# Performance work log

Hardware: AMD Instinct MI355X
Metric: run time of the kernel (lower is better)

The kernel has to match this reference:

```python
import jax, jax.numpy as jnp
import numpy as np

EPS = 1e-7          # keras backend epsilon
BN_EPS = 1e-3       # keras BatchNormalization default epsilon
SCALES = (2, 4, 8, 16, 32)  # 2**i for i in 1..max_scale, max_scale=5


def _box_filter(x, k):
    # depthwise conv with all-ones k x k kernel, SAME padding (TF semantics)
    c = x.shape[-1]
    kern = jnp.ones((k, k, 1, c), x.dtype)
    return jax.lax.conv_general_dilated(
        x, kern, (1, 1), 'SAME',
        dimension_numbers=('NHWC', 'HWIO', 'NHWC'),
        feature_group_count=c)


def setup_inputs() -> dict:
    key = jax.random.key(0)
    ks = jax.random.split(key, 4)
    B, H, W, C, R = 16, 56, 56, 128, 8
    x = jax.random.normal(ks[0], (B, H, W, C), jnp.float32)
    kappa = jax.random.uniform(ks[1], (len(SCALES),), jnp.float32, -0.5, 0.5)
    W1 = jax.random.normal(ks[2], (C, C // R), jnp.float32) * (1.0 / np.sqrt(C))
    b1 = jnp.zeros((C // R,), jnp.float32)
    W2 = jax.random.normal(ks[3], (C // R, C), jnp.float32) * (1.0 / np.sqrt(C // R))
    b2 = jnp.zeros((C,), jnp.float32)
    gamma = jnp.ones((C,), jnp.float32)
    beta = jnp.zeros((C,), jnp.float32)
    bn_mean = jnp.zeros((C,), jnp.float32)
    bn_var = jnp.ones((C,), jnp.float32)
    return dict(x=x, kappa=kappa, W1=W1, b1=b1, W2=W2, b2=b2,
                gamma=gamma, beta=beta, bn_mean=bn_mean, bn_var=bn_var)


def reference(x, kappa, W1, b1, W2, b2, gamma, beta, bn_mean, bn_var):
    # per-sample min-max scaling over (H, W, C)
    xmin = jnp.min(x, axis=(1, 2, 3), keepdims=True)
    xmax = jnp.max(x, axis=(1, 2, 3), keepdims=True)
    xs = (x - xmin) / (xmax - xmin + EPS)

    # multi-scale box measures: [B,H,W,C,S]
    measures = jnp.stack([_box_filter(xs, k) for k in SCALES], axis=-1)
    log_m = jnp.log(measures + EPS)
    log_r = jnp.log(jnp.asarray(SCALES, jnp.float32))  # [S]

    # OLS slope of log_m vs log_r along scale axis -> alphas [B,H,W,C]
    xc = log_r - jnp.mean(log_r)
    alphas = jnp.sum(log_m * xc, axis=-1) / jnp.sum(xc * xc)

    # squeeze-and-excite on alphas
    squeeze = jnp.mean(alphas, axis=(1, 2))            # [B,C]
    hidden = jax.nn.relu(squeeze @ W1 + b1)            # [B,C//r]
    excite = jax.nn.sigmoid(hidden @ W2 + b2)          # [B,C]

    # weighted OLS estimate: alpha * (log_k + log_r) -> [B,H,W,C,S]
    k_ = jax.nn.sigmoid(kappa)
    log_k = jax.nn.sigmoid(jnp.log(k_ + EPS))          # [S]
    wols = alphas[..., None] * (log_k + log_r)

    # standardized (mean-centered) cosine similarity along scale axis, in [0,1]
    a = log_m - jnp.mean(log_m, axis=-1, keepdims=True)
    b = wols - jnp.mean(wols, axis=-1, keepdims=True)
    cos = jnp.sum(a * b, axis=-1) / (
        jnp.linalg.norm(a, axis=-1) * jnp.linalg.norm(b, axis=-1) + EPS)
    sim = 0.5 * (cos + 1.0)                            # [B,H,W,C]

    # inference-mode batchnorm on alphas
    alpha_norm = gamma * (alphas - bn_mean) * jax.lax.rsqrt(bn_var + BN_EPS) + beta

    x_exc = xs * excite[:, None, None, :]
    return sim * jax.nn.sigmoid(alpha_norm) + (1.0 - sim) * x_exc
```

## Files before the change

kernel.cpp:

```cpp
#include <hip/hip_runtime.h>
#include <hip/hip_fp16.h>

#define NTOT   6422528
#define NPERB  401408
#define NQ4    100352
#define LOG2E  1.4426950408889634f

__device__ __forceinline__ float sigmoidf_fast(float x) {
    return __builtin_amdgcn_rcpf(1.f + __expf(-x));
}

__device__ __forceinline__ void kappa_consts(const float* kap, float* dcs) {
    float v[5]; float mean = 0.f;
    for (int s = 0; s < 5; s++) {
        float lr = 0.6931471805599453f * (float)(s + 1);
        float k_ = 1.f / (1.f + expf(-kap[s]));
        float lk = 1.f / (1.f + expf(-logf(k_ + 1e-7f)));
        v[s] = lk + lr; mean += v[s];
    }
    mean *= 0.2f; float nd = 0.f;
    for (int s = 0; s < 5; s++) { float d = v[s] - mean; dcs[s] = d; nd += d * d; }
    dcs[5] = sqrtf(nd);
}

struct ScaleU { int rb1, rb0; float xmch; };

__global__ void k_minmax(const float4* __restrict__ x4,
                         float* __restrict__ pmxp, float* __restrict__ pmnp,
                         float* __restrict__ sq) {
    int p = blockIdx.x;
    int b = p & 15, chunk = p >> 4;
    if (chunk == 0) {
        for (int k = threadIdx.x; k < 128; k += 256) sq[b * 128 + k] = 0.f;
    }
    const float4* base = x4 + b * NQ4 + chunk * 1568;
    float mx = -3.4e38f, mn = 3.4e38f;
    for (int q = threadIdx.x; q < 1568; q += 256) {
        float4 v = base[q];
        mx = fmaxf(mx, fmaxf(fmaxf(v.x, v.y), fmaxf(v.z, v.w)));
        mn = fminf(mn, fminf(fminf(v.x, v.y), fminf(v.z, v.w)));
    }
    __shared__ float rmx[4], rmn[4];
    int lane = threadIdx.x & 63, w = threadIdx.x >> 6;
#pragma unroll
    for (int off = 32; off; off >>= 1) {
        mx = fmaxf(mx, __shfl_down(mx, off));
        mn = fminf(mn, __shfl_down(mn, off));
    }
    if (lane == 0) { rmx[w] = mx; rmn[w] = mn; }
    __syncthreads();
    if (threadIdx.x == 0) {
        mx = fmaxf(fmaxf(rmx[0], rmx[1]), fmaxf(rmx[2], rmx[3]));
        mn = fminf(fminf(rmn[0], rmn[1]), fminf(rmn[2], rmn[3]));
        pmxp[b * 64 + chunk] = mx;
        pmnp[b * 64 + chunk] = mn;
    }
}

__launch_bounds__(448, 7)
__global__ void k_satg(const float* __restrict__ x,   const float* __restrict__ kap,
                       const float* __restrict__ gam, const float* __restrict__ bet,
                       const float* __restrict__ bnm, const float* __restrict__ bnv,
                       const float* __restrict__ pmxp, const float* __restrict__ pmnp,
                       float* __restrict__ sq, unsigned int* __restrict__ ABu) {
    __shared__ float2 SAT2[57 * 57];
    __shared__ float2 tot2[448];
    __shared__ float  wsum[14];
    __shared__ float  cst[9];

    const int p = blockIdx.x;
    const int b = p & 15, cg = p >> 4;
    const int c0 = cg * 2;
    const int t = threadIdx.x;
    const int pos = t % 56;
    const int seg = t / 56;

    if (t < 57) SAT2[t] = make_float2(0.f, 0.f);
    if (t >= 64 && t < 120) SAT2[(t - 63) * 57] = make_float2(0.f, 0.f);
    if (t == 128) {
        float d[6]; kappa_consts(kap, d);
#pragma unroll
        for (int s2 = 0; s2 < 6; s2++) cst[s2] = d[s2];
    }

    float2 v[7];
    {
        const float2* xp = (const float2*)(x + b * NPERB + seg * 7 * 7168 + pos * 128 + c0);
        float2 acc = make_float2(0.f, 0.f);
#pragma unroll
        for (int k = 0; k < 7; k++) {
            float2 xv = xp[k * 3584];
            acc.x += xv.x; acc.y += xv.y;
            v[k] = acc;
        }
        tot2[t] = acc;
    }
    __syncthreads();
    if (t < 64) {
        float mxv = pmxp[b * 64 + t];
        float mnv = pmnp[b * 64 + t];
#pragma unroll
        for (int off = 32; off; off >>= 1) {
            mxv = fmaxf(mxv, __shfl_down(mxv, off));
            mnv = fminf(mnv, __shfl_down(mnv, off));
        }
        if (t == 0) {
            float xi = 1.f / (mxv - mnv + 1e-7f);
            cst[6] = mnv; cst[7] = xi; cst[8] = mnv * xi;
        }
    }
    {
        float2 base = make_float2(0.f, 0.f);
        for (int s = 0; s < seg; s++) {
            float2 tv = tot2[s * 56 + pos];
            base.x += tv.x; base.y += tv.y;
        }
#pragma unroll
        for (int k = 0; k < 7; k++)
            SAT2[(seg * 7 + 1 + k) * 57 + (pos + 1)] =
                make_float2(base.x + v[k].x, base.y + v[k].y);
    }
    __syncthreads();

    {
        const int rbase = (pos + 1) * 57 + seg * 7 + 1;
#pragma unroll
        for (int k = 0; k < 7; k++) v[k] = SAT2[rbase + k];
#pragma unroll
        for (int k = 1; k < 7; k++) { v[k].x += v[k - 1].x; v[k].y += v[k - 1].y; }
        tot2[seg * 56 + pos] = v[6];
    }
    __syncthreads();
    {
        float2 base = make_float2(0.f, 0.f);
        for (int s = 0; s < seg; s++) {
            float2 tv = tot2[s * 56 + pos];
            base.x += tv.x; base.y += tv.y;
        }
        const int rbase = (pos + 1) * 57 + seg * 7 + 1;
#pragma unroll
        for (int k = 0; k < 7; k++)
            SAT2[rbase + k] = make_float2(base.x + v[k].x, base.y + v[k].y);
    }
    __syncthreads();

    float asx = 0.f, asy = 0.f;
    {
        const int i = pos;
        const int j0 = seg * 7;
        const float xm = cst[6], xi = cst[7], xmxi = cst[8];
        const float d0 = cst[0], d1 = cst[1], d2 = cst[2], d3 = cst[3], d4 = cst[4], nd = cst[5];
        float C1x, C0x, C1y, C0y;
        {
            float g = gam[c0], be = bet[c0], bm = bnm[c0];
            float rsv = rsqrtf(bnv[c0] + 1e-3f);
            C1x = -(g * rsv) * (LOG2E * 0.1f);
            C0x = -(be - g * bm * rsv) * LOG2E;
            g = gam[c0 + 1]; be = bet[c0 + 1]; bm = bnm[c0 + 1];
            rsv = rsqrtf(bnv[c0 + 1] + 1e-3f);
            C1y = -(g * rsv) * (LOG2E * 0.1f);
            C0y = -(be - g * bm * rsv) * LOG2E;
        }

        auto mkU = [&](int hk) {
            ScaleU uu;
            int y1g = min(i + hk, 55) + 1;
            int y0g = max(i - hk + 1, 0);
            uu.rb1 = y1g * 57; uu.rb0 = y0g * 57;
            uu.xmch = xm * (float)(y1g - y0g);
            return uu;
        };
        const ScaleU u0 = mkU(1), u1 = mkU(2), u2 = mkU(4), u3 = mkU(8), u4 = mkU(16);

        auto meas = [&](int j, const ScaleU& uu, int hk) -> float2 {
            int x1g = min(j + hk, 55) + 1;
            int x0g = max(j - hk + 1, 0);
            float cw = (float)(x1g - x0g);
            float2 a = SAT2[uu.rb1 + x1g], bq = SAT2[uu.rb0 + x1g];
            float2 cq = SAT2[uu.rb1 + x0g], dq = SAT2[uu.rb0 + x0g];
            float sx = a.x - bq.x - cq.x + dq.x;
            float sy = a.y - bq.y - cq.y + dq.y;
            float tx = fmaf(-uu.xmch, cw, sx);
            float ty = fmaf(-uu.xmch, cw, sy);
            float2 r;
            r.x = __log2f(fmaxf(fmaf(tx, xi, 1e-7f), 1e-7f));
            r.y = __log2f(fmaxf(fmaf(ty, xi, 1e-7f), 1e-7f));
            return r;
        };

        const float2* xrow = (const float2*)(x + b * NPERB + i * 7168 + c0);
        uint2* abrow = (uint2*)(ABu + b * NPERB + i * 7168 + c0);
#pragma unroll 2
        for (int jj = 0; jj < 7; jj++) {
            int j = j0 + jj;
            float2 l0 = meas(j, u0, 1);
            float2 l1 = meas(j, u1, 2);
            float2 l2 = meas(j, u2, 4);
            float2 l3 = meas(j, u3, 8);
            float2 l4 = meas(j, u4, 16);
            float2 xv = xrow[j * 64];
            uint2 outw;
            {
                float w2 = -2.f * l0.x - l1.x + l3.x + 2.f * l4.x;
                asx += w2;
                float alphas = w2 * 0.1f;
                float mean = 0.2f * (l0.x + l1.x + l2.x + l3.x + l4.x);
                float a0 = l0.x - mean, a1 = l1.x - mean, a2 = l2.x - mean,
                      a3 = l3.x - mean, a4 = l4.x - mean;
                float na2  = a0 * a0 + a1 * a1 + a2 * a2 + a3 * a3 + a4 * a4;
                float adot = a0 * d0 + a1 * d1 + a2 * d2 + a3 * d3 + a4 * d4;
                float na = __builtin_amdgcn_sqrtf(na2);
                float cosv = (alphas * adot) *
                             __builtin_amdgcn_rcpf(na * fabsf(alphas) * nd + 1e-7f);
                float sim = 0.5f * (cosv + 1.f);
                float sbn = __builtin_amdgcn_rcpf(1.f + exp2f(C1x * w2 + C0x));
                float xs = fmaf(xv.x, xi, -xmxi);
                outw.x = __builtin_bit_cast(unsigned int,
                          __floats2half2_rn(sim * sbn, (1.f - sim) * xs));
            }
            {
                float w2 = -2.f * l0.y - l1.y + l3.y + 2.f * l4.y;
                asy += w2;
                float alphas = w2 * 0.1f;
                float mean = 0.2f * (l0.y + l1.y + l2.y + l3.y + l4.y);
                float a0 = l0.y - mean, a1 = l1.y - mean, a2 = l2.y - mean,
                      a3 = l3.y - mean, a4 = l4.y - mean;
                float na2  = a0 * a0 + a1 * a1 + a2 * a2 + a3 * a3 + a4 * a4;
                float adot = a0 * d0 + a1 * d1 + a2 * d2 + a3 * d3 + a4 * d4;
                float na = __builtin_amdgcn_sqrtf(na2);
                float cosv = (alphas * adot) *
                             __builtin_amdgcn_rcpf(na * fabsf(alphas) * nd + 1e-7f);
                float sim = 0.5f * (cosv + 1.f);
                float sbn = __builtin_amdgcn_rcpf(1.f + exp2f(C1y * w2 + C0y));
                float xs = fmaf(xv.y, xi, -xmxi);
                outw.y = __builtin_bit_cast(unsigned int,
                          __floats2half2_rn(sim * sbn, (1.f - sim) * xs));
            }
            abrow[j * 64] = outw;
        }
    }
#pragma unroll
    for (int off = 32; off; off >>= 1) {
        asx += __shfl_down(asx, off);
        asy += __shfl_down(asy, off);
    }
    if ((t & 63) == 0) { wsum[(t >> 6) * 2] = asx; wsum[(t >> 6) * 2 + 1] = asy; }
    __syncthreads();
    if (t < 2) {
        float s = 0.f;
#pragma unroll
        for (int w = 0; w < 7; w++) s += wsum[w * 2 + t];
        atomicAdd(&sq[b * 128 + c0 + t], s * 0.1f);
    }
}

__launch_bounds__(256)
__global__ void k_mix(const unsigned int* __restrict__ ABu, const float* __restrict__ sq,
                      const float* __restrict__ W1, const float* __restrict__ b1,
                      const float* __restrict__ W2, const float* __restrict__ b2,
                      float* __restrict__ out) {
    __shared__ float sqz[128];
    __shared__ float hidp[256];
    __shared__ float hid[16];
    __shared__ float exc[128];
    int p = blockIdx.x;
    int b = p & 15, chunk = p >> 4;
    int tid = threadIdx.x;
    if (tid < 128) sqz[tid] = sq[b * 128 + tid] * (1.f / 3136.f);
    __syncthreads();
    {
        int h = tid & 15, g = tid >> 4;
        float acc = 0.f;
#pragma unroll
        for (int k = 0; k < 8; k++) {
            int c2 = g * 8 + k;
            acc += sqz[c2] * W1[c2 * 16 + h];
        }
        hidp[tid] = acc;
    }
    __syncthreads();
    if (tid < 16) {
        float acc = b1[tid];
#pragma unroll
        for (int g = 0; g < 16; g++) acc += hidp[g * 16 + tid];
        hid[tid] = fmaxf(acc, 0.f);
    }
    __syncthreads();
    if (tid < 128) {
        float acc = b2[tid];
#pragma unroll
        for (int h = 0; h < 16; h++) acc += hid[h] * W2[h * 128 + tid];
        exc[tid] = sigmoidf_fast(acc);
    }
    __syncthreads();
    const uint4* ab4 = (const uint4*)ABu + b * NQ4 + chunk * 784;
    float4* out4 = (float4*)out + b * NQ4 + chunk * 784;
    for (int q = tid; q < 784; q += 256) {
        int cb = ((chunk * 784 + q) & 31) << 2;
        uint4 u = ab4[q];
        float2 p0 = __half22float2(__builtin_bit_cast(__half2, u.x));
        float2 p1 = __half22float2(__builtin_bit_cast(__half2, u.y));
        float2 p2 = __half22float2(__builtin_bit_cast(__half2, u.z));
        float2 p3 = __half22float2(__builtin_bit_cast(__half2, u.w));
        out4[q] = make_float4(p0.x + p0.y * exc[cb],
                              p1.x + p1.y * exc[cb + 1],
                              p2.x + p2.y * exc[cb + 2],
                              p3.x + p3.y * exc[cb + 3]);
    }
}

extern "C" void kernel_launch(void* const* d_in, const int* in_sizes, int n_in,
                              void* d_out, int out_size, void* d_ws, size_t ws_size,
                              hipStream_t stream) {
    const float* x   = (const float*)d_in[0];
    const float* kap = (const float*)d_in[1];
    const float* W1  = (const float*)d_in[2];
    const float* b1  = (const float*)d_in[3];
    const float* W2  = (const float*)d_in[4];
    const float* b2  = (const float*)d_in[5];
    const float* gam = (const float*)d_in[6];
    const float* bet = (const float*)d_in[7];
    const float* bnm = (const float*)d_in[8];
    const float* bnv = (const float*)d_in[9];
    float* out = (float*)d_out;

    float* sq   = (float*)d_ws;
    float* pmxp = sq + 2048;
    float* pmnp = pmxp + 1024;
    unsigned* ABu = (unsigned*)(pmnp + 1024);

    k_minmax<<<1024, 256, 0, stream>>>((const float4*)x, pmxp, pmnp, sq);
    k_satg<<<1024, 448, 0, stream>>>(x, kap, gam, bet, bnm, bnv, pmxp, pmnp, sq, ABu);
    k_mix<<<2048, 256, 0, stream>>>(ABu, sq, W1, b1, W2, b2, out);
}
```

Baseline: 143.1 us.

## Transpose intermediate buffer to channel-pair-major layout and recover x from SAT

The intermediate half2 buffer is stored channel-pair-major with pixels ordered column-major, so k_satg's per-thread stores become contiguous across threads. The input value is reconstructed from the shared-memory summed-area table instead of being reloaded from global memory with a large stride. k_mix now gathers from two channel-pair planes per output float4, which makes its reads strided. Reconstructing x from prefix-sum differences may also lose float precision.

Result: no change. 145.7 us (+1.8%).

```diff
diff --git a/kernel.cpp b/kernel.cpp
--- a/kernel.cpp
+++ b/kernel.cpp
@@ -62,7 +62,7 @@
                        const float* __restrict__ gam, const float* __restrict__ bet,
                        const float* __restrict__ bnm, const float* __restrict__ bnv,
                        const float* __restrict__ pmxp, const float* __restrict__ pmnp,
-                       float* __restrict__ sq, unsigned int* __restrict__ ABu) {
+                       float* __restrict__ sq, uint2* __restrict__ ABp) {
     __shared__ float2 SAT2[57 * 57];
     __shared__ float2 tot2[448];
     __shared__ float  wsum[14];
@@ -148,7 +148,8 @@
     {
         const int i = pos;
         const int j0 = seg * 7;
-        const float xm = cst[6], xi = cst[7], xmxi = cst[8];
+        const float xi = cst[7], xmxi = cst[8];
+        const float xm = cst[6];
         const float d0 = cst[0], d1 = cst[1], d2 = cst[2], d3 = cst[3], d4 = cst[4], nd = cst[5];
         float C1x, C0x, C1y, C0y;
         {
@@ -171,6 +172,7 @@
             return uu;
         };
         const ScaleU u0 = mkU(1), u1 = mkU(2), u2 = mkU(4), u3 = mkU(8), u4 = mkU(16);
+        const int rb1x = (i + 1) * 57, rb0x = i * 57;
 
         auto meas = [&](int j, const ScaleU& uu, int hk) -> float2 {
             int x1g = min(j + hk, 55) + 1;
@@ -188,9 +190,7 @@
             return r;
         };
 
-        const float2* xrow = (const float2*)(x + b * NPERB + i * 7168 + c0);
-        uint2* abrow = (uint2*)(ABu + b * NPERB + i * 7168 + c0);
-#pragma unroll 2
+        uint2* abp = ABp + (b * 64 + cg) * 3136 + i;
         for (int jj = 0; jj < 7; jj++) {
             int j = j0 + jj;
             float2 l0 = meas(j, u0, 1);
@@ -198,7 +198,10 @@
             float2 l2 = meas(j, u2, 4);
             float2 l3 = meas(j, u3, 8);
             float2 l4 = meas(j, u4, 16);
-            float2 xv = xrow[j * 64];
+            float2 aX = SAT2[rb1x + j + 1], bX = SAT2[rb0x + j + 1];
+            float2 cX = SAT2[rb1x + j],     dX = SAT2[rb0x + j];
+            float xvx = aX.x - bX.x - cX.x + dX.x;
+            float xvy = aX.y - bX.y - cX.y + dX.y;
             uint2 outw;
             {
                 float w2 = -2.f * l0.x - l1.x + l3.x + 2.f * l4.x;
@@ -214,7 +217,7 @@
                              __builtin_amdgcn_rcpf(na * fabsf(alphas) * nd + 1e-7f);
                 float sim = 0.5f * (cosv + 1.f);
                 float sbn = __builtin_amdgcn_rcpf(1.f + exp2f(C1x * w2 + C0x));
-                float xs = fmaf(xv.x, xi, -xmxi);
+                float xs = fmaf(xvx, xi, -xmxi);
                 outw.x = __builtin_bit_cast(unsigned int,
                           __floats2half2_rn(sim * sbn, (1.f - sim) * xs));
             }
@@ -232,11 +235,11 @@
                              __builtin_amdgcn_rcpf(na * fabsf(alphas) * nd + 1e-7f);
                 float sim = 0.5f * (cosv + 1.f);
                 float sbn = __builtin_amdgcn_rcpf(1.f + exp2f(C1y * w2 + C0y));
-                float xs = fmaf(xv.y, xi, -xmxi);
+                float xs = fmaf(xvy, xi, -xmxi);
                 outw.y = __builtin_bit_cast(unsigned int,
                           __floats2half2_rn(sim * sbn, (1.f - sim) * xs));
             }
-            abrow[j * 64] = outw;
+            abp[j * 56] = outw;
         }
     }
 #pragma unroll
@@ -255,7 +258,7 @@
 }
 
 __launch_bounds__(256)
-__global__ void k_mix(const unsigned int* __restrict__ ABu, const float* __restrict__ sq,
+__global__ void k_mix(const uint2* __restrict__ ABp, const float* __restrict__ sq,
                       const float* __restrict__ W1, const float* __restrict__ b1,
                       const float* __restrict__ W2, const float* __restrict__ b2,
                       float* __restrict__ out) {
@@ -293,15 +296,21 @@
         exc[tid] = sigmoidf_fast(acc);
     }
     __syncthreads();
-    const uint4* ab4 = (const uint4*)ABu + b * NQ4 + chunk * 784;
+    const uint2* base_b = ABp + b * 64 * 3136;
     float4* out4 = (float4*)out + b * NQ4 + chunk * 784;
     for (int q = tid; q < 784; q += 256) {
-        int cb = ((chunk * 784 + q) & 31) << 2;
-        uint4 u = ab4[q];
-        float2 p0 = __half22float2(__builtin_bit_cast(__half2, u.x));
-        float2 p1 = __half22float2(__builtin_bit_cast(__half2, u.y));
-        float2 p2 = __half22float2(__builtin_bit_cast(__half2, u.z));
-        float2 p3 = __half22float2(__builtin_bit_cast(__half2, u.w));
+        int local = chunk * 784 + q;
+        int pix = local >> 5;
+        int c4 = local & 31;
+        int i = pix / 56, j = pix % 56;
+        int poff = j * 56 + i;
+        uint2 r0 = base_b[(c4 * 2    ) * 3136 + poff];
+        uint2 r1 = base_b[(c4 * 2 + 1) * 3136 + poff];
+        float2 p0 = __half22float2(__builtin_bit_cast(__half2, r0.x));
+        float2 p1 = __half22float2(__builtin_bit_cast(__half2, r0.y));
+        float2 p2 = __half22float2(__builtin_bit_cast(__half2, r1.x));
+        float2 p3 = __half22float2(__builtin_bit_cast(__half2, r1.y));
+        int cb = c4 << 2;
         out4[q] = make_float4(p0.x + p0.y * exc[cb],
                               p1.x + p1.y * exc[cb + 1],
                               p2.x + p2.y * exc[cb + 2],
@@ -327,9 +336,9 @@
     float* sq   = (float*)d_ws;
     float* pmxp = sq + 2048;
     float* pmnp = pmxp + 1024;
-    unsigned* ABu = (unsigned*)(pmnp + 1024);
+    uint2* ABp  = (uint2*)(pmnp + 1024);
 
     k_minmax<<<1024, 256, 0, stream>>>((const float4*)x, pmxp, pmnp, sq);
-    k_satg<<<1024, 448, 0, stream>>>(x, kap, gam, bet, bnm, bnv, pmxp, pmnp, sq, ABu);
-    k_mix<<<2048, 256, 0, stream>>>(ABu, sq, W1, b1, W2, b2, out);
-}
+    k_satg<<<1024, 448, 0, stream>>>(x, kap, gam, bet, bnm, bnv, pmxp, pmnp, sq, ABp);
+    k_mix<<<2048, 256, 0, stream>>>(ABp, sq, W1, b1, W2, b2, out);
+}
```
